# Kernel optimization log

Measured on AMD Instinct MI355X. Metric: run time of the kernel, lower is better.

## Reference

```python
import jax, jax.numpy as jnp
import numpy as np

T = 2_000_000  # timesteps


def setup_inputs() -> dict:
    key = jax.random.key(0)
    u = jax.random.normal(key, (T, 2), dtype=jnp.float32) * 10.0  # external forces per step
    x0 = jnp.zeros((4,), dtype=jnp.float32)  # [z1, v1, z2, v2]
    c = jnp.array([10.0, 10.0, 10.0], dtype=jnp.float32)   # trainable damping c1,c2,c3
    m = jnp.array([20.0, 10.0], dtype=jnp.float32)          # masses m1,m2 (frozen)
    k = jnp.array([2.0e3, 1.0e3, 5.0e3], dtype=jnp.float32) # stiffness k1,k2,k3 (frozen)
    dt = jnp.float32(0.002)
    return {"u": u, "x0": x0, "c": c, "m": m, "k": k, "dt": dt}


def reference(u, x0, c, m, k, dt):
    c1, c2, c3 = c[0], c[1], c[2]
    m1, m2 = m[0], m[1]
    k1, k2, k3 = k[0], k[1], k[2]

    def deriv(x, ut):
        # x = [z1, v1, z2, v2]; returns dx/dt = [v1, a1, v2, a2]
        z1, v1, z2, v2 = x[0], x[1], x[2], x[3]
        a1 = (ut[0] - (c1 + c2) * v1 + c2 * v2 - (k1 + k2) * z1 + k2 * z2) / m1
        a2 = (ut[1] - (c3 + c2) * v2 + c2 * v1 - (k3 + k2) * z2 + k2 * z1) / m2
        return jnp.stack([v1, a1, v2, a2])

    half = dt * 0.5

    def step(x, ut):
        s1 = deriv(x, ut)
        s2 = deriv(x + half * s1, ut)
        s3 = deriv(x + half * s2, ut)
        s4 = deriv(x + dt * s3, ut)
        xn = x + (dt / 6.0) * (s1 + 2.0 * s2 + 2.0 * s3 + s4)
        y = jnp.stack([xn[0], xn[2]])  # positions z1, z2 (matches cell output)
        return xn, y

    _, ys = jax.lax.scan(step, x0, u)
    return ys  # [T, 2]
```

## Files before the change

### kernel.cpp

```cpp
#include <hip/hip_runtime.h>

#define BLK 128
#define LS  32
#define SPB (BLK*LS)
#define MID_T 512

#define WS_M   0
#define WS_N   16
#define WS_SK  24
#define WS_GK  152
#define WS_RES 320

#define STEP4(Mx,Nx, s0,s1,s2,s3, ux,uy, n0,n1,n2,n3)                                              \
  n0 = fmaf(Mx[0],s0,  fmaf(Mx[1],s1,  fmaf(Mx[2],s2,  fmaf(Mx[3],s3,  fmaf(Nx[0],ux, Nx[1]*uy))))); \
  n1 = fmaf(Mx[4],s0,  fmaf(Mx[5],s1,  fmaf(Mx[6],s2,  fmaf(Mx[7],s3,  fmaf(Nx[2],ux, Nx[3]*uy))))); \
  n2 = fmaf(Mx[8],s0,  fmaf(Mx[9],s1,  fmaf(Mx[10],s2, fmaf(Mx[11],s3, fmaf(Nx[4],ux, Nx[5]*uy))))); \
  n3 = fmaf(Mx[12],s0, fmaf(Mx[13],s1, fmaf(Mx[14],s2, fmaf(Mx[15],s3, fmaf(Nx[6],ux, Nx[7]*uy)))));

__device__ __forceinline__ float4 aff_apply(const float* Mx, float4 l, float4 c) {
  float4 r;
  r.x = fmaf(Mx[0],l.x,  fmaf(Mx[1],l.y,  fmaf(Mx[2],l.z,  fmaf(Mx[3],l.w,  c.x))));
  r.y = fmaf(Mx[4],l.x,  fmaf(Mx[5],l.y,  fmaf(Mx[6],l.z,  fmaf(Mx[7],l.w,  c.y))));
  r.z = fmaf(Mx[8],l.x,  fmaf(Mx[9],l.y,  fmaf(Mx[10],l.z, fmaf(Mx[11],l.w, c.z))));
  r.w = fmaf(Mx[12],l.x, fmaf(Mx[13],l.y, fmaf(Mx[14],l.z, fmaf(Mx[15],l.w, c.w))));
  return r;
}

__device__ __forceinline__ void mm4d(const double* X, const double* Y, double* Z) {
  for (int i = 0; i < 4; ++i)
    for (int j = 0; j < 4; ++j) {
      double s = 0.0;
      for (int l = 0; l < 4; ++l) s += X[i*4+l] * Y[l*4+j];
      Z[i*4+j] = s;
    }
}

__global__ void k_setup(const float* __restrict__ cin, const float* __restrict__ min_,
                        const float* __restrict__ kin, const float* __restrict__ dtin,
                        float* __restrict__ ws) {
  double c1 = cin[0], c2 = cin[1], c3 = cin[2];
  double m1 = min_[0], m2 = min_[1];
  double k1 = kin[0], k2 = kin[1], k3 = kin[2];
  double h  = dtin[0];

  double A[16] = { 0.0, 1.0, 0.0, 0.0,
                  -(k1+k2)/m1, -(c1+c2)/m1,  k2/m1,  c2/m1,
                   0.0, 0.0, 0.0, 1.0,
                   k2/m2,  c2/m2, -(k3+k2)/m2, -(c3+c2)/m2 };

  double Q[16], R[16], S[16], M[16], tmp[16];
  for (int i = 0; i < 16; ++i) Q[i] = ((i % 5 == 0) ? 1.0 : 0.0) + (h/4.0)*A[i];
  mm4d(A, Q, tmp);
  for (int i = 0; i < 16; ++i) R[i] = ((i % 5 == 0) ? 1.0 : 0.0) + (h/3.0)*tmp[i];
  mm4d(A, R, tmp);
  for (int i = 0; i < 16; ++i) S[i] = ((i % 5 == 0) ? 1.0 : 0.0) + (h/2.0)*tmp[i];
  mm4d(A, S, tmp);
  for (int i = 0; i < 16; ++i) M[i] = ((i % 5 == 0) ? 1.0 : 0.0) + h*tmp[i];

  double N[8];
  for (int i = 0; i < 4; ++i) {
    N[2*i+0] = h * S[i*4+1] / m1;
    N[2*i+1] = h * S[i*4+3] / m2;
  }

  for (int i = 0; i < 16; ++i) ws[WS_M+i] = (float)M[i];
  for (int i = 0; i < 8;  ++i) ws[WS_N+i] = (float)N[i];

  double P[16]; for (int i = 0; i < 16; ++i) P[i] = M[i];
  for (int r = 0; r < 5; ++r) { mm4d(P, P, tmp); for (int i = 0; i < 16; ++i) P[i] = tmp[i]; }

  for (int i = 0; i < 16; ++i) ws[WS_SK+i] = (float)P[i];
  for (int k = 1; k < 8; ++k) {
    mm4d(P, P, tmp); for (int i = 0; i < 16; ++i) P[i] = tmp[i];
    for (int i = 0; i < 16; ++i) ws[WS_SK+16*k+i] = (float)P[i];
  }
  for (int i = 0; i < 16; ++i) ws[WS_GK+i] = (float)P[i];
  for (int k = 1; k < 9; ++k) {
    mm4d(P, P, tmp); for (int i = 0; i < 16; ++i) P[i] = tmp[i];
    for (int i = 0; i < 16; ++i) ws[WS_GK+16*k+i] = (float)P[i];
  }
}

__launch_bounds__(BLK)
__global__ void k_pass1(const float4* __restrict__ u4, const float* __restrict__ ws,
                        float4* __restrict__ bout, float4* __restrict__ aggout, int T2) {
  __shared__ float2 tile[BLK * 33];
  __shared__ float4 S1[BLK];
  __shared__ float  SKs[8*16];
  const int tid   = threadIdx.x;
  const int base2 = blockIdx.x * SPB;

  float Mm[16], Nn[8];
  #pragma unroll
  for (int i = 0; i < 16; ++i) Mm[i] = ws[WS_M+i];
  #pragma unroll
  for (int i = 0; i < 8;  ++i) Nn[i] = ws[WS_N+i];
  if (tid < 128) SKs[tid] = ws[WS_SK + tid];

  #pragma unroll
  for (int kk = 0; kk < LS/2; ++kk) {
    int idx4 = tid + kk*BLK;
    int p0 = base2 + 2*idx4;
    float4 v = make_float4(0.f, 0.f, 0.f, 0.f);
    if (p0 < T2) v = u4[(base2 >> 1) + idx4];
    int l = 2*idx4, r = l >> 5, e = l & 31;
    tile[r*33 + e]     = make_float2(v.x, v.y);
    tile[r*33 + e + 1] = make_float2(v.z, v.w);
  }
  __syncthreads();

  float b0 = 0.f, b1 = 0.f, b2 = 0.f, b3 = 0.f;
  #pragma unroll
  for (int j = 0; j < LS; ++j) {
    float2 uu = tile[tid*33 + j];
    float n0, n1, n2, n3;
    STEP4(Mm, Nn, b0, b1, b2, b3, uu.x, uu.y, n0, n1, n2, n3);
    b0 = n0; b1 = n1; b2 = n2; b3 = n3;
  }
  float4 b = make_float4(b0, b1, b2, b3);
  bout[blockIdx.x * BLK + tid] = b;

  S1[tid] = b;
  __syncthreads();
  for (int k = 0; k < 7; ++k) {
    int off = 1 << k;
    float4 l, c;
    bool act = (tid >= off);
    if (act) { l = S1[tid - off]; c = S1[tid]; }
    __syncthreads();
    if (act) S1[tid] = aff_apply(&SKs[16*k], l, c);
    __syncthreads();
  }
  if (tid == BLK-1) aggout[blockIdx.x] = S1[BLK-1];
}

__launch_bounds__(MID_T)
__global__ void k_mid(const float* __restrict__ ws, float4* __restrict__ agg,
                      const float* __restrict__ x0in, int nblk) {
  __shared__ float4 A[MID_T];
  __shared__ float  GKs[9*16];
  const int t = threadIdx.x;
  const int n = nblk + 1;

  if (t < 144) GKs[t] = ws[WS_GK + t];
  if (t == 0)      A[0] = make_float4(x0in[0], x0in[1], x0in[2], x0in[3]);
  else if (t < n)  A[t] = agg[t-1];
  __syncthreads();

  for (int k = 0; k < 9; ++k) {
    int off = 1 << k;
    if (off >= n) break;
    float4 l, c;
    bool act = (t >= off && t < n);
    if (act) { l = A[t - off]; c = A[t]; }
    __syncthreads();
    if (act) A[t] = aff_apply(&GKs[16*k], l, c);
    __syncthreads();
  }
  if (t < nblk) agg[t] = A[t];
}

__launch_bounds__(BLK)
__global__ void k_pass3(const float4* __restrict__ u4, const float* __restrict__ ws,
                        const float4* __restrict__ bbuf, const float4* __restrict__ xbs,
                        float4* __restrict__ out4, int T2) {
  __shared__ float2 tile[BLK * 33];
  __shared__ float4 S3[BLK + 1];
  __shared__ float  SKs[8*16];
  const int tid   = threadIdx.x;
  const int base2 = blockIdx.x * SPB;

  float Mm[16], Nn[8];
  #pragma unroll
  for (int i = 0; i < 16; ++i) Mm[i] = ws[WS_M+i];
  #pragma unroll
  for (int i = 0; i < 8;  ++i) Nn[i] = ws[WS_N+i];
  if (tid < 128) SKs[tid] = ws[WS_SK + tid];

  #pragma unroll
  for (int kk = 0; kk < LS/2; ++kk) {
    int idx4 = tid + kk*BLK;
    int p0 = base2 + 2*idx4;
    float4 v = make_float4(0.f, 0.f, 0.f, 0.f);
    if (p0 < T2) v = u4[(base2 >> 1) + idx4];
    int l = 2*idx4, r = l >> 5, e = l & 31;
    tile[r*33 + e]     = make_float2(v.x, v.y);
    tile[r*33 + e + 1] = make_float2(v.z, v.w);
  }

  if (tid == 0) S3[0] = xbs[blockIdx.x];
  S3[tid + 1] = bbuf[blockIdx.x * BLK + tid];
  __syncthreads();

  for (int k = 0; k < 8; ++k) {
    int off = 1 << k;
    int i = tid + 1;
    float4 l, c;
    bool act = (i >= off);
    if (act) { l = S3[i - off]; c = S3[i]; }
    __syncthreads();
    if (act) S3[i] = aff_apply(&SKs[16*k], l, c);
    __syncthreads();
  }

  float4 xs = S3[tid];
  float x0 = xs.x, x1 = xs.y, x2 = xs.z, x3 = xs.w;
  #pragma unroll
  for (int j = 0; j < LS; ++j) {
    float2 uu = tile[tid*33 + j];
    float n0, n1, n2, n3;
    STEP4(Mm, Nn, x0, x1, x2, x3, uu.x, uu.y, n0, n1, n2, n3);
    x0 = n0; x1 = n1; x2 = n2; x3 = n3;
    tile[tid*33 + j] = make_float2(x0, x2);
  }
  __syncthreads();

  #pragma unroll
  for (int kk = 0; kk < LS/2; ++kk) {
    int idx4 = tid + kk*BLK;
    int p0 = base2 + 2*idx4;
    if (p0 < T2) {
      int l = 2*idx4, r = l >> 5, e = l & 31;
      float2 a = tile[r*33 + e];
      float2 b = tile[r*33 + e + 1];
      out4[(base2 >> 1) + idx4] = make_float4(a.x, a.y, b.x, b.y);
    }
  }
}

extern "C" void kernel_launch(void* const* d_in, const int* in_sizes, int n_in,
                              void* d_out, int out_size, void* d_ws, size_t ws_size,
                              hipStream_t stream) {
  const float* u   = (const float*)d_in[0];
  const float* x0  = (const float*)d_in[1];
  const float* cc  = (const float*)d_in[2];
  const float* mm  = (const float*)d_in[3];
  const float* kk  = (const float*)d_in[4];
  const float* dt  = (const float*)d_in[5];

  const int T2     = in_sizes[0] / 2;
  const int nblk   = (T2 + SPB - 1) / SPB;
  const int nchunk = nblk * BLK;

  float*  ws   = (float*)d_ws;
  float4* bbuf = (float4*)(ws + WS_RES);
  float4* abuf = bbuf + nchunk;

  k_setup<<<1, 1, 0, stream>>>(cc, mm, kk, dt, ws);
  k_pass1<<<nblk, BLK, 0, stream>>>((const float4*)u, ws, bbuf, abuf, T2);
  k_mid  <<<1, MID_T, 0, stream>>>(ws, abuf, x0, nblk);
  k_pass3<<<nblk, BLK, 0, stream>>>((const float4*)u, ws, bbuf, abuf, (float4*)d_out, T2);
}
```

Before: 104.0 us.

## Fuse three scan passes into one kernel with grid-wide atomic handoff

Merges pass1, the middle block-level scan and pass3 into a single kernel. Blocks publish their aggregates and bump an atomic counter. Block 0 spins until all aggregates arrive, scans them and releases a flag, while the other blocks spin on that flag. Each thread then rebuilds its starting state from the block prefix and its in-block exclusive scan, using matrix powers, instead of re-scanning. This removes two launches, the second read of u and the bbuf round trip. It relies on all blocks (about 489) being co-resident, since otherwise the spin-waits could deadlock.

Measured after the change: 162.5 us. 1.56x slower.

```diff
diff --git a/kernel.cpp b/kernel.cpp
--- a/kernel.cpp
+++ b/kernel.cpp
@@ -3,13 +3,13 @@
 #define BLK 128
 #define LS  32
 #define SPB (BLK*LS)
-#define MID_T 512
 
 #define WS_M   0
 #define WS_N   16
 #define WS_SK  24
 #define WS_GK  152
-#define WS_RES 320
+#define WS_CNT 320
+#define WS_AGG 336
 
 #define STEP4(Mx,Nx, s0,s1,s2,s3, ux,uy, n0,n1,n2,n3)                                              \
   n0 = fmaf(Mx[0],s0,  fmaf(Mx[1],s1,  fmaf(Mx[2],s2,  fmaf(Mx[3],s3,  fmaf(Nx[0],ux, Nx[1]*uy))))); \
@@ -24,6 +24,10 @@
   r.z = fmaf(Mx[8],l.x,  fmaf(Mx[9],l.y,  fmaf(Mx[10],l.z, fmaf(Mx[11],l.w, c.z))));
   r.w = fmaf(Mx[12],l.x, fmaf(Mx[13],l.y, fmaf(Mx[14],l.z, fmaf(Mx[15],l.w, c.w))));
   return r;
+}
+
+__device__ __forceinline__ float4 matvec(const float* Mx, float4 v) {
+  return aff_apply(Mx, v, make_float4(0.f, 0.f, 0.f, 0.f));
 }
 
 __device__ __forceinline__ void mm4d(const double* X, const double* Y, double* Z) {
@@ -79,16 +83,31 @@
     mm4d(P, P, tmp); for (int i = 0; i < 16; ++i) P[i] = tmp[i];
     for (int i = 0; i < 16; ++i) ws[WS_GK+16*k+i] = (float)P[i];
   }
+
+  int* cnt = (int*)(ws + WS_CNT);
+  cnt[0] = 0;
+  cnt[1] = 0;
 }
 
 __launch_bounds__(BLK)
-__global__ void k_pass1(const float4* __restrict__ u4, const float* __restrict__ ws,
-                        float4* __restrict__ bout, float4* __restrict__ aggout, int T2) {
+__global__ void k_fused(const float4* __restrict__ u4, float* __restrict__ ws,
+                        const float* __restrict__ x0in, float4* __restrict__ out4,
+                        int T2, int nblk) {
   __shared__ float2 tile[BLK * 33];
   __shared__ float4 S1[BLK];
   __shared__ float  SKs[8*16];
+  __shared__ float  GKs[9*16];
+  __shared__ float4 MA[512];
+  __shared__ float4 MB[512];
+  __shared__ float4 Xsh;
+
   const int tid   = threadIdx.x;
-  const int base2 = blockIdx.x * SPB;
+  const int bid   = blockIdx.x;
+  const int base2 = bid * SPB;
+
+  int*    cnt1 = (int*)(ws + WS_CNT);
+  int*    cnt2 = (int*)(ws + WS_CNT) + 1;
+  float4* agg  = (float4*)(ws + WS_AGG);
 
   float Mm[16], Nn[8];
   #pragma unroll
@@ -96,6 +115,8 @@
   #pragma unroll
   for (int i = 0; i < 8;  ++i) Nn[i] = ws[WS_N+i];
   if (tid < 128) SKs[tid] = ws[WS_SK + tid];
+  if (tid < 16)  { GKs[tid] = ws[WS_GK + tid]; GKs[tid+16] = ws[WS_GK + tid + 16]; }
+  if (tid >= 16 && tid < 128) GKs[tid + 16] = ws[WS_GK + tid + 16];
 
   #pragma unroll
   for (int kk = 0; kk < LS/2; ++kk) {
@@ -117,11 +138,10 @@
     STEP4(Mm, Nn, b0, b1, b2, b3, uu.x, uu.y, n0, n1, n2, n3);
     b0 = n0; b1 = n1; b2 = n2; b3 = n3;
   }
-  float4 b = make_float4(b0, b1, b2, b3);
-  bout[blockIdx.x * BLK + tid] = b;
-
-  S1[tid] = b;
-  __syncthreads();
+  S1[tid] = make_float4(b0, b1, b2, b3);
+  __syncthreads();
+
+  #pragma unroll
   for (int k = 0; k < 7; ++k) {
     int off = 1 << k;
     float4 l, c;
@@ -131,80 +151,72 @@
     if (act) S1[tid] = aff_apply(&SKs[16*k], l, c);
     __syncthreads();
   }
-  if (tid == BLK-1) aggout[blockIdx.x] = S1[BLK-1];
-}
-
-__launch_bounds__(MID_T)
-__global__ void k_mid(const float* __restrict__ ws, float4* __restrict__ agg,
-                      const float* __restrict__ x0in, int nblk) {
-  __shared__ float4 A[MID_T];
-  __shared__ float  GKs[9*16];
-  const int t = threadIdx.x;
-  const int n = nblk + 1;
-
-  if (t < 144) GKs[t] = ws[WS_GK + t];
-  if (t == 0)      A[0] = make_float4(x0in[0], x0in[1], x0in[2], x0in[3]);
-  else if (t < n)  A[t] = agg[t-1];
-  __syncthreads();
-
-  for (int k = 0; k < 9; ++k) {
-    int off = 1 << k;
-    if (off >= n) break;
-    float4 l, c;
-    bool act = (t >= off && t < n);
-    if (act) { l = A[t - off]; c = A[t]; }
-    __syncthreads();
-    if (act) A[t] = aff_apply(&GKs[16*k], l, c);
-    __syncthreads();
-  }
-  if (t < nblk) agg[t] = A[t];
-}
-
-__launch_bounds__(BLK)
-__global__ void k_pass3(const float4* __restrict__ u4, const float* __restrict__ ws,
-                        const float4* __restrict__ bbuf, const float4* __restrict__ xbs,
-                        float4* __restrict__ out4, int T2) {
-  __shared__ float2 tile[BLK * 33];
-  __shared__ float4 S3[BLK + 1];
-  __shared__ float  SKs[8*16];
-  const int tid   = threadIdx.x;
-  const int base2 = blockIdx.x * SPB;
-
-  float Mm[16], Nn[8];
-  #pragma unroll
-  for (int i = 0; i < 16; ++i) Mm[i] = ws[WS_M+i];
-  #pragma unroll
-  for (int i = 0; i < 8;  ++i) Nn[i] = ws[WS_N+i];
-  if (tid < 128) SKs[tid] = ws[WS_SK + tid];
-
-  #pragma unroll
-  for (int kk = 0; kk < LS/2; ++kk) {
-    int idx4 = tid + kk*BLK;
-    int p0 = base2 + 2*idx4;
-    float4 v = make_float4(0.f, 0.f, 0.f, 0.f);
-    if (p0 < T2) v = u4[(base2 >> 1) + idx4];
-    int l = 2*idx4, r = l >> 5, e = l & 31;
-    tile[r*33 + e]     = make_float2(v.x, v.y);
-    tile[r*33 + e + 1] = make_float2(v.z, v.w);
-  }
-
-  if (tid == 0) S3[0] = xbs[blockIdx.x];
-  S3[tid + 1] = bbuf[blockIdx.x * BLK + tid];
-  __syncthreads();
-
-  for (int k = 0; k < 8; ++k) {
-    int off = 1 << k;
-    int i = tid + 1;
-    float4 l, c;
-    bool act = (i >= off);
-    if (act) { l = S3[i - off]; c = S3[i]; }
-    __syncthreads();
-    if (act) S3[i] = aff_apply(&SKs[16*k], l, c);
-    __syncthreads();
-  }
-
-  float4 xs = S3[tid];
-  float x0 = xs.x, x1 = xs.y, x2 = xs.z, x3 = xs.w;
+
+  if (tid == BLK-1) {
+    agg[bid] = S1[BLK-1];
+    __threadfence();
+    __hip_atomic_fetch_add(cnt1, 1, __ATOMIC_RELEASE, __HIP_MEMORY_SCOPE_AGENT);
+  }
+
+  if (bid == 0) {
+    if (tid == 0) {
+      while (__hip_atomic_load(cnt1, __ATOMIC_ACQUIRE, __HIP_MEMORY_SCOPE_AGENT) < nblk)
+        __builtin_amdgcn_s_sleep(2);
+    }
+    __syncthreads();
+
+    const int n = nblk + 1;
+    #pragma unroll
+    for (int j = 0; j < 4; ++j) {
+      int i = tid + BLK*j;
+      if (i < n) MA[i] = (i == 0) ? make_float4(x0in[0], x0in[1], x0in[2], x0in[3])
+                                  : agg[i-1];
+    }
+    __syncthreads();
+
+    float4* Aa = MA; float4* Bb = MB;
+    for (int k = 0; k < 9; ++k) {
+      int off = 1 << k;
+      if (off >= n) break;
+      #pragma unroll
+      for (int j = 0; j < 4; ++j) {
+        int i = tid + BLK*j;
+        if (i < n) {
+          float4 v = Aa[i];
+          if (i >= off) v = aff_apply(&GKs[16*k], Aa[i-off], v);
+          Bb[i] = v;
+        }
+      }
+      __syncthreads();
+      float4* t = Aa; Aa = Bb; Bb = t;
+    }
+
+    #pragma unroll
+    for (int j = 0; j < 4; ++j) {
+      int i = tid + BLK*j;
+      if (i < nblk) agg[i] = Aa[i];
+    }
+    __syncthreads();
+    if (tid == 0) {
+      __threadfence();
+      __hip_atomic_store(cnt2, 1, __ATOMIC_RELEASE, __HIP_MEMORY_SCOPE_AGENT);
+    }
+  }
+
+  if (tid == 0) {
+    while (__hip_atomic_load(cnt2, __ATOMIC_ACQUIRE, __HIP_MEMORY_SCOPE_AGENT) < 1)
+      __builtin_amdgcn_s_sleep(2);
+    Xsh = agg[bid];
+  }
+  __syncthreads();
+
+  float4 v = Xsh;
+  #pragma unroll
+  for (int k = 0; k < 7; ++k)
+    if (tid & (1 << k)) v = matvec(&SKs[16*k], v);
+  float4 p = (tid > 0) ? S1[tid-1] : make_float4(0.f, 0.f, 0.f, 0.f);
+  float x0 = v.x + p.x, x1 = v.y + p.y, x2 = v.z + p.z, x3 = v.w + p.w;
+
   #pragma unroll
   for (int j = 0; j < LS; ++j) {
     float2 uu = tile[tid*33 + j];
@@ -238,16 +250,10 @@
   const float* kk  = (const float*)d_in[4];
   const float* dt  = (const float*)d_in[5];
 
-  const int T2     = in_sizes[0] / 2;
-  const int nblk   = (T2 + SPB - 1) / SPB;
-  const int nchunk = nblk * BLK;
-
-  float*  ws   = (float*)d_ws;
-  float4* bbuf = (float4*)(ws + WS_RES);
-  float4* abuf = bbuf + nchunk;
+  const int T2   = in_sizes[0] / 2;
+  const int nblk = (T2 + SPB - 1) / SPB;
+  float* ws = (float*)d_ws;
 
   k_setup<<<1, 1, 0, stream>>>(cc, mm, kk, dt, ws);
-  k_pass1<<<nblk, BLK, 0, stream>>>((const float4*)u, ws, bbuf, abuf, T2);
-  k_mid  <<<1, MID_T, 0, stream>>>(ws, abuf, x0, nblk);
-  k_pass3<<<nblk, BLK, 0, stream>>>((const float4*)u, ws, bbuf, abuf, (float4*)d_out, T2);
-}
+  k_fused<<<nblk, BLK, 0, stream>>>((const float4*)u, ws, x0, (float4*)d_out, T2, nblk);
+}
```
